# Kernel tuning notes

Hardware: AMD Instinct MI355X
Metric: run time of the kernel (lower is better)

Reference implementation:

```python
import jax, jax.numpy as jnp
import numpy as np

NUM_TRIPLES = 16_000_000  # N: training triples in the buffer
NUM_NEG = 65_536          # B: proposed negative triples
NUM_IDS = 100_000         # shared id range for heads/relations/tails


def setup_inputs() -> dict:
    key = jax.random.key(0)
    k_neg, k_mt = jax.random.split(key)
    negative_batch = jax.random.randint(k_neg, (NUM_NEG, 3), 0, NUM_IDS, dtype=jnp.int32)
    mapped_triples = jax.random.randint(k_mt, (NUM_TRIPLES, 3), 0, NUM_IDS, dtype=jnp.int32)
    return {"negative_batch": negative_batch, "mapped_triples": mapped_triples}


def _in_sorted(values, sorted_ref):
    """membership test: values[i] in sorted_ref (sorted 1-D array)."""
    idx = jnp.clip(jnp.searchsorted(sorted_ref, values), 0, sorted_ref.shape[0] - 1)
    return sorted_ref[idx] == values


def reference(negative_batch, mapped_triples):
    # Torch original: head_filter[n] = any_b(mt[n,0] == neg[b,0]); same for relation
    # on the head-filtered subset; final_filter[b] = any surviving triple with
    # mt[n,2] == neg[b,2]. Boolean-indexing of mapped_triples is replaced by a
    # mask (identical math, static shapes); O(B*N) broadcast compares replaced by
    # sort + searchsorted membership (same result, far less traffic).
    neg_heads_sorted = jnp.sort(negative_batch[:, 0])
    neg_rels_sorted = jnp.sort(negative_batch[:, 1])
    # [N] bool: triple's head matches ANY negative head AND relation matches ANY negative relation
    surviving = _in_sorted(mapped_triples[:, 0], neg_heads_sorted) & _in_sorted(
        mapped_triples[:, 1], neg_rels_sorted
    )
    # tails of surviving triples; -1 sentinel never matches (ids are >= 0).
    # Empty-survivor case (the torch RuntimeError branch) falls out naturally.
    tails = jnp.where(surviving, mapped_triples[:, 2], jnp.int32(-1))
    tails_sorted = jnp.sort(tails)
    final_filter = _in_sorted(negative_batch[:, 2], tails_sorted)  # [B] bool
    keep_mask = ~final_filter
    # torch returns negative_batch[keep_mask] (data-dependent shape); under jit we
    # return the same rows with filtered rows set to -1, plus the keep mask.
    filtered_negative_batch = jnp.where(keep_mask[:, None], negative_batch, jnp.int32(-1))
    return filtered_negative_batch, keep_mask
```

## Files before the change

### kernel.cpp

```cpp
#include <hip/hip_runtime.h>
#include <stdint.h>

#define NWORDS 3125
#define NWP    3136
#define NVEC   (NWP / 4)
#define SCAN_BLOCKS 1024
#define SCAN_THREADS 512
#define NCHUNK 32
#define CHUNK  (SCAN_BLOCKS / NCHUNK)

__global__ void zero_ws_kernel(uint32_t* __restrict__ w, int n) {
    int i = blockIdx.x * blockDim.x + threadIdx.x;
    if (i < n) w[i] = 0u;
}

__global__ void build_hr_kernel(const int* __restrict__ neg, int B,
                                uint32_t* __restrict__ headb,
                                uint32_t* __restrict__ relb) {
    int b = blockIdx.x * blockDim.x + threadIdx.x;
    if (b >= B) return;
    int h = neg[b * 3 + 0];
    int r = neg[b * 3 + 1];
    atomicOr(&headb[h >> 5], 1u << (h & 31));
    atomicOr(&relb[r >> 5], 1u << (r & 31));
}

#define PROC(A, B_, C_) do {                                                   \
    int hs[4] = {(A).x, (A).w, (B_).z, (C_).y};                                \
    int rs[4] = {(A).y, (B_).x, (B_).w, (C_).z};                               \
    int ts[4] = {(A).z, (B_).y, (C_).x, (C_).w};                               \
    _Pragma("unroll")                                                          \
    for (int k = 0; k < 4; ++k) {                                              \
        uint32_t hbit = (sh[hs[k] >> 5] >> (hs[k] & 31)) & 1u;                 \
        uint32_t rbit = (sr[rs[k] >> 5] >> (rs[k] & 31)) & 1u;                 \
        if (hbit & rbit) {                                                     \
            int t = ts[k];                                                     \
            uint32_t bit = 1u << (t & 31);                                     \
            if (!(st[t >> 5] & bit)) atomicOr(&st[t >> 5], bit);               \
        }                                                                      \
    }                                                                          \
} while (0)

__global__ __launch_bounds__(SCAN_THREADS, 8) void scan_triples_kernel(
        const int* __restrict__ mt, int N,
        const uint32_t* __restrict__ headb,
        const uint32_t* __restrict__ relb,
        uint32_t* __restrict__ copies) {
    __shared__ __align__(16) uint32_t sh[NWP];
    __shared__ __align__(16) uint32_t sr[NWP];
    __shared__ __align__(16) uint32_t st[NWP];

    uint4* sh4 = (uint4*)sh;
    uint4* sr4 = (uint4*)sr;
    uint4* st4 = (uint4*)st;
    const uint4* hb4 = (const uint4*)headb;
    const uint4* rb4 = (const uint4*)relb;
    for (int i = threadIdx.x; i < NVEC; i += blockDim.x) {
        sh4[i] = hb4[i];
        sr4[i] = rb4[i];
        st4[i] = make_uint4(0u, 0u, 0u, 0u);
    }
    __syncthreads();

    const int tid = blockIdx.x * blockDim.x + threadIdx.x;
    const int stride = gridDim.x * blockDim.x;
    const int ngroups = N >> 2;
    const int4* __restrict__ mt4 = (const int4*)mt;

    int g = tid;
    for (; g + stride < ngroups; g += 2 * stride) {
        size_t b0 = (size_t)g * 3;
        size_t b1 = (size_t)(g + stride) * 3;
        int4 a0 = mt4[b0 + 0], a1 = mt4[b0 + 1], a2 = mt4[b0 + 2];
        int4 d0 = mt4[b1 + 0], d1 = mt4[b1 + 1], d2 = mt4[b1 + 2];
        PROC(a0, a1, a2);
        PROC(d0, d1, d2);
    }
    for (; g < ngroups; g += stride) {
        size_t b0 = (size_t)g * 3;
        int4 a0 = mt4[b0 + 0], a1 = mt4[b0 + 1], a2 = mt4[b0 + 2];
        PROC(a0, a1, a2);
    }
    int base = ngroups << 2;
    for (int i = base + tid; i < N; i += stride) {
        int h = mt[i * 3 + 0], r = mt[i * 3 + 1], t = mt[i * 3 + 2];
        if (((sh[h >> 5] >> (h & 31)) & 1u) && ((sr[r >> 5] >> (r & 31)) & 1u)) {
            uint32_t bit = 1u << (t & 31);
            if (!(st[t >> 5] & bit)) atomicOr(&st[t >> 5], bit);
        }
    }

    __syncthreads();
    uint4* dst4 = (uint4*)(copies + (size_t)blockIdx.x * NWP);
    for (int i = threadIdx.x; i < NVEC; i += blockDim.x) dst4[i] = st4[i];
}

__global__ void reduce_tails_kernel(const uint32_t* __restrict__ copies,
                                    uint32_t* __restrict__ partials) {
    int idx = blockIdx.x * blockDim.x + threadIdx.x;
    if (idx >= NCHUNK * NVEC) return;
    int i  = idx % NVEC;
    int ch = idx / NVEC;
    const uint4* c4 = (const uint4*)copies;
    uint4 acc = make_uint4(0u, 0u, 0u, 0u);
    int c0 = ch * CHUNK;
    for (int c = 0; c < CHUNK; ++c) {
        uint4 v = c4[(size_t)(c0 + c) * NVEC + i];
        acc.x |= v.x; acc.y |= v.y; acc.z |= v.z; acc.w |= v.w;
    }
    ((uint4*)partials)[(size_t)ch * NVEC + i] = acc;
}

__global__ void finalize_kernel(const int* __restrict__ neg, int B,
                                const uint32_t* __restrict__ partials,
                                int* __restrict__ out) {
    int b = blockIdx.x * blockDim.x + threadIdx.x;
    if (b >= B) return;
    int h = neg[b * 3 + 0];
    int r = neg[b * 3 + 1];
    int t = neg[b * 3 + 2];
    int w = t >> 5;
    uint32_t acc = 0u;
#pragma unroll
    for (int c = 0; c < NCHUNK; ++c) acc |= partials[(size_t)c * NWP + w];
    bool filtered = (acc >> (t & 31)) & 1u;
    int keep = filtered ? 0 : 1;
    out[b * 3 + 0] = keep ? h : -1;
    out[b * 3 + 1] = keep ? r : -1;
    out[b * 3 + 2] = keep ? t : -1;
    out[3 * B + b] = keep;
}

extern "C" void kernel_launch(void* const* d_in, const int* in_sizes, int n_in,
                              void* d_out, int out_size, void* d_ws, size_t ws_size,
                              hipStream_t stream) {
    const int* neg = (const int*)d_in[0];
    const int* mt  = (const int*)d_in[1];
    int B = in_sizes[0] / 3;
    int N = in_sizes[1] / 3;
    int* out = (int*)d_out;

    uint32_t* ws       = (uint32_t*)d_ws;
    uint32_t* headb    = ws;
    uint32_t* relb     = ws + NWP;
    uint32_t* partials = ws + 2 * NWP;
    uint32_t* copies   = ws + (2 + NCHUNK) * NWP;

    zero_ws_kernel<<<(2 * NWP + 255) / 256, 256, 0, stream>>>(ws, 2 * NWP);
    build_hr_kernel<<<(B + 255) / 256, 256, 0, stream>>>(neg, B, headb, relb);
    scan_triples_kernel<<<SCAN_BLOCKS, SCAN_THREADS, 0, stream>>>(
        mt, N, headb, relb, copies);
    {
        int total = NCHUNK * NVEC;
        reduce_tails_kernel<<<(total + 255) / 256, 256, 0, stream>>>(copies, partials);
    }
    finalize_kernel<<<(B + 255) / 256, 256, 0, stream>>>(neg, B, partials, out);
}
```

Before: 61.30 us.

## Use per-triple overlapping 16B loads, memset zeroing, and two-stage tail reduction

The scan loop now processes one triple per thread with an unaligned 16-byte load at offset 12*i, replacing the 4-triple, 3×int4 grouped loads. The last triple is handled separately so the load never reads past the buffer. The zero kernel becomes hipMemsetAsync, and the final OR over 32 chunk partials moves into a separate reduceB kernel, so finalize does one lookup instead of 32. This trades aligned vector loads for simpler per-thread work, reads a third more bytes, and adds one extra launch.

```diff
diff --git a/kernel.cpp b/kernel.cpp
--- a/kernel.cpp
+++ b/kernel.cpp
@@ -9,10 +9,7 @@
 #define NCHUNK 32
 #define CHUNK  (SCAN_BLOCKS / NCHUNK)
 
-__global__ void zero_ws_kernel(uint32_t* __restrict__ w, int n) {
-    int i = blockIdx.x * blockDim.x + threadIdx.x;
-    if (i < n) w[i] = 0u;
-}
+typedef int4 __attribute__((aligned(4))) int4_a4;
 
 __global__ void build_hr_kernel(const int* __restrict__ neg, int B,
                                 uint32_t* __restrict__ headb,
@@ -24,22 +21,6 @@
     atomicOr(&headb[h >> 5], 1u << (h & 31));
     atomicOr(&relb[r >> 5], 1u << (r & 31));
 }
-
-#define PROC(A, B_, C_) do {                                                   \
-    int hs[4] = {(A).x, (A).w, (B_).z, (C_).y};                                \
-    int rs[4] = {(A).y, (B_).x, (B_).w, (C_).z};                               \
-    int ts[4] = {(A).z, (B_).y, (C_).x, (C_).w};                               \
-    _Pragma("unroll")                                                          \
-    for (int k = 0; k < 4; ++k) {                                              \
-        uint32_t hbit = (sh[hs[k] >> 5] >> (hs[k] & 31)) & 1u;                 \
-        uint32_t rbit = (sr[rs[k] >> 5] >> (rs[k] & 31)) & 1u;                 \
-        if (hbit & rbit) {                                                     \
-            int t = ts[k];                                                     \
-            uint32_t bit = 1u << (t & 31);                                     \
-            if (!(st[t >> 5] & bit)) atomicOr(&st[t >> 5], bit);               \
-        }                                                                      \
-    }                                                                          \
-} while (0)
 
 __global__ __launch_bounds__(SCAN_THREADS, 8) void scan_triples_kernel(
         const int* __restrict__ mt, int N,
@@ -62,32 +43,26 @@
     }
     __syncthreads();
 
-    const int tid = blockIdx.x * blockDim.x + threadIdx.x;
-    const int stride = gridDim.x * blockDim.x;
-    const int ngroups = N >> 2;
-    const int4* __restrict__ mt4 = (const int4*)mt;
+    const uint32_t tid = blockIdx.x * blockDim.x + threadIdx.x;
+    const uint32_t stride = gridDim.x * blockDim.x;
+    const char* __restrict__ base = (const char*)mt;
 
-    int g = tid;
-    for (; g + stride < ngroups; g += 2 * stride) {
-        size_t b0 = (size_t)g * 3;
-        size_t b1 = (size_t)(g + stride) * 3;
-        int4 a0 = mt4[b0 + 0], a1 = mt4[b0 + 1], a2 = mt4[b0 + 2];
-        int4 d0 = mt4[b1 + 0], d1 = mt4[b1 + 1], d2 = mt4[b1 + 2];
-        PROC(a0, a1, a2);
-        PROC(d0, d1, d2);
-    }
-    for (; g < ngroups; g += stride) {
-        size_t b0 = (size_t)g * 3;
-        int4 a0 = mt4[b0 + 0], a1 = mt4[b0 + 1], a2 = mt4[b0 + 2];
-        PROC(a0, a1, a2);
-    }
-    int base = ngroups << 2;
-    for (int i = base + tid; i < N; i += stride) {
-        int h = mt[i * 3 + 0], r = mt[i * 3 + 1], t = mt[i * 3 + 2];
-        if (((sh[h >> 5] >> (h & 31)) & 1u) && ((sr[r >> 5] >> (r & 31)) & 1u)) {
+    for (uint32_t i = tid; i < (uint32_t)(N - 1); i += stride) {
+        int4 v = *(const int4_a4*)(base + i * 12u);
+        int h = v.x, r = v.y, t = v.z;
+        uint32_t hbit = (sh[h >> 5] >> (h & 31)) & 1u;
+        uint32_t rbit = (sr[r >> 5] >> (r & 31)) & 1u;
+        if (hbit & rbit) {
             uint32_t bit = 1u << (t & 31);
             if (!(st[t >> 5] & bit)) atomicOr(&st[t >> 5], bit);
         }
+    }
+    if (tid == 0) {
+        int h = mt[(size_t)(N - 1) * 3 + 0];
+        int r = mt[(size_t)(N - 1) * 3 + 1];
+        int t = mt[(size_t)(N - 1) * 3 + 2];
+        if (((sh[h >> 5] >> (h & 31)) & 1u) && ((sr[r >> 5] >> (r & 31)) & 1u))
+            atomicOr(&st[t >> 5], 1u << (t & 31));
     }
 
     __syncthreads();
@@ -95,8 +70,8 @@
     for (int i = threadIdx.x; i < NVEC; i += blockDim.x) dst4[i] = st4[i];
 }
 
-__global__ void reduce_tails_kernel(const uint32_t* __restrict__ copies,
-                                    uint32_t* __restrict__ partials) {
+__global__ void reduceA_kernel(const uint32_t* __restrict__ copies,
+                               uint32_t* __restrict__ partials) {
     int idx = blockIdx.x * blockDim.x + threadIdx.x;
     if (idx >= NCHUNK * NVEC) return;
     int i  = idx % NVEC;
@@ -111,19 +86,25 @@
     ((uint4*)partials)[(size_t)ch * NVEC + i] = acc;
 }
 
+__global__ void reduceB_kernel(const uint32_t* __restrict__ partials,
+                               uint32_t* __restrict__ final_b) {
+    int w = blockIdx.x * blockDim.x + threadIdx.x;
+    if (w >= NWP) return;
+    uint32_t acc = 0u;
+#pragma unroll
+    for (int c = 0; c < NCHUNK; ++c) acc |= partials[c * NWP + w];
+    final_b[w] = acc;
+}
+
 __global__ void finalize_kernel(const int* __restrict__ neg, int B,
-                                const uint32_t* __restrict__ partials,
+                                const uint32_t* __restrict__ final_b,
                                 int* __restrict__ out) {
     int b = blockIdx.x * blockDim.x + threadIdx.x;
     if (b >= B) return;
     int h = neg[b * 3 + 0];
     int r = neg[b * 3 + 1];
     int t = neg[b * 3 + 2];
-    int w = t >> 5;
-    uint32_t acc = 0u;
-#pragma unroll
-    for (int c = 0; c < NCHUNK; ++c) acc |= partials[(size_t)c * NWP + w];
-    bool filtered = (acc >> (t & 31)) & 1u;
+    bool filtered = (final_b[t >> 5] >> (t & 31)) & 1u;
     int keep = filtered ? 0 : 1;
     out[b * 3 + 0] = keep ? h : -1;
     out[b * 3 + 1] = keep ? r : -1;
@@ -143,16 +124,18 @@
     uint32_t* ws       = (uint32_t*)d_ws;
     uint32_t* headb    = ws;
     uint32_t* relb     = ws + NWP;
-    uint32_t* partials = ws + 2 * NWP;
-    uint32_t* copies   = ws + (2 + NCHUNK) * NWP;
+    uint32_t* final_b  = ws + 2 * NWP;
+    uint32_t* partials = ws + 3 * NWP;
+    uint32_t* copies   = ws + (3 + NCHUNK) * NWP;
 
-    zero_ws_kernel<<<(2 * NWP + 255) / 256, 256, 0, stream>>>(ws, 2 * NWP);
+    hipMemsetAsync(ws, 0, 2 * NWP * sizeof(uint32_t), stream);
     build_hr_kernel<<<(B + 255) / 256, 256, 0, stream>>>(neg, B, headb, relb);
     scan_triples_kernel<<<SCAN_BLOCKS, SCAN_THREADS, 0, stream>>>(
         mt, N, headb, relb, copies);
     {
         int total = NCHUNK * NVEC;
-        reduce_tails_kernel<<<(total + 255) / 256, 256, 0, stream>>>(copies, partials);
+        reduceA_kernel<<<(total + 255) / 256, 256, 0, stream>>>(copies, partials);
     }
-    finalize_kernel<<<(B + 255) / 256, 256, 0, stream>>>(neg, B, partials, out);
+    reduceB_kernel<<<(NWP + 255) / 256, 256, 0, stream>>>(partials, final_b);
+    finalize_kernel<<<(B + 255) / 256, 256, 0, stream>>>(neg, B, final_b, out);
 }
```

After: 57.20 us. 1.07x faster.
